# Kernel tuning notes

Hardware: AMD Instinct MI355X
Metric: run time of the kernel (lower is better)

Reference implementation:

```python
import jax, jax.numpy as jnp
import numpy as np

EPS = 1e-6

def rms_norm(x, w):
    x32 = x.astype(jnp.float32)
    y = x32 * jax.lax.rsqrt(jnp.mean(x32 * x32, axis=-1, keepdims=True) + EPS)
    return y.astype(x.dtype) * w

def setup_inputs() -> dict:
    key = jax.random.key(0)
    ks = jax.random.split(key, 12)
    V, Dm, S, Bz, L = 32000, 1024, 256, 2, 2048
    input_ids = jax.random.randint(ks[0], (Bz, L), 0, V)
    embedding = 0.02 * jax.random.normal(ks[1], (V, Dm), dtype=jnp.float32)
    embed_norm_w = jnp.ones((Dm,), dtype=jnp.float32)
    ssm_norm_w = jnp.ones((Dm,), dtype=jnp.float32)
    # A = 0.999 * exp(1j * theta): magnitude 0.999, random phase
    theta = jax.random.normal(ks[2], (S,), dtype=jnp.float32)
    A_re = 0.999 * jnp.cos(theta)
    A_im = 0.999 * jnp.sin(theta)
    # complex randn has real/imag parts with std 1/sqrt(2)
    cs = 1.0 / np.sqrt(2.0)
    B_re = cs * jax.random.normal(ks[3], (Dm, S), dtype=jnp.float32) / np.sqrt(S)
    B_im = cs * jax.random.normal(ks[4], (Dm, S), dtype=jnp.float32) / np.sqrt(S)
    C_re = cs * jax.random.normal(ks[5], (S, Dm), dtype=jnp.float32) / np.sqrt(S)
    C_im = cs * jax.random.normal(ks[6], (S, Dm), dtype=jnp.float32) / np.sqrt(S)
    D_p = jax.random.normal(ks[7], (Dm,), dtype=jnp.float32)
    head_w = jax.random.normal(ks[8], (Dm, V), dtype=jnp.float32) / np.sqrt(Dm)
    head_b = jnp.zeros((V,), dtype=jnp.float32)
    return dict(input_ids=input_ids, embedding=embedding, embed_norm_w=embed_norm_w,
                ssm_norm_w=ssm_norm_w, A_re=A_re, A_im=A_im, B_re=B_re, B_im=B_im,
                C_re=C_re, C_im=C_im, D_p=D_p, head_w=head_w, head_b=head_b)

def reference(input_ids, embedding, embed_norm_w, ssm_norm_w, A_re, A_im,
              B_re, B_im, C_re, C_im, D_p, head_w, head_b):
    # embed + RMSNorm
    x = rms_norm(embedding[input_ids], embed_norm_w)      # [B, L, D]
    # SSM input norm
    u = rms_norm(x, ssm_norm_w)                           # [B, L, D]
    L = u.shape[1]
    A = (A_re + 1j * A_im).astype(jnp.complex64)          # [S]
    Bc = (B_re + 1j * B_im).astype(jnp.complex64)         # [D, S]
    Cc = (C_re + 1j * C_im).astype(jnp.complex64)         # [S, D]
    # per-channel geometric kernel A^t, t = 0..L-1
    t = jnp.arange(L)[:, None]
    A_powers = A[None, :] ** t                            # [L, S] complex64
    uB = jnp.einsum('bli,iz->blz', u.astype(jnp.complex64), Bc)  # [B, L, S]
    # FFT-based causal convolution (fast_conv)
    T = 1 << int(np.ceil(np.log2(2 * L - 1)))
    Af = jnp.fft.fft(A_powers, n=T, axis=0)               # [T, S]
    Uf = jnp.fft.fft(uB, n=T, axis=1)                     # [B, T, S]
    xs = jnp.fft.ifft(Af[None, :, :] * Uf, axis=1)[:, :L]  # [B, L, S]
    y = jnp.real(jnp.einsum('blz,zo->blo', xs, Cc)) + D_p  # [B, L, D]
    return y @ head_w + head_b                            # [B, L, V]
```

## Files before the change

### kernel.cpp

```cpp
#include <hip/hip_runtime.h>

static __device__ __forceinline__ unsigned short f2bf(float f) {
  union { float f; unsigned u; } v; v.f = f;
  unsigned r = v.u + 0x7fffu + ((v.u >> 16) & 1u);
  return (unsigned short)(r >> 16);
}

struct alignas(8) us4 { unsigned short x, y, z, w; };

typedef __bf16 bf16x8 __attribute__((ext_vector_type(8)));
typedef float f32x4 __attribute__((ext_vector_type(4)));

static __device__ __forceinline__ void load_lds16(const void* g, void* l) {
  __builtin_amdgcn_global_load_lds(
      (const __attribute__((address_space(1))) unsigned int*)g,
      (__attribute__((address_space(3))) unsigned int*)l,
      16, 0, 0);
}

static __device__ __forceinline__ float block_sum(float v, float* sred) {
  #pragma unroll
  for (int o = 32; o > 0; o >>= 1) v += __shfl_down(v, o, 64);
  const int tid = threadIdx.x;
  __syncthreads();
  if ((tid & 63) == 0) sred[tid >> 6] = v;
  __syncthreads();
  return sred[0] + sred[1] + sred[2] + sred[3];
}

__global__ __launch_bounds__(256) void embed_norm(
    const int* __restrict__ ids, const float* __restrict__ emb,
    const float* __restrict__ w1, const float* __restrict__ w2,
    unsigned short* __restrict__ u_bf)
{
  __shared__ float sred[4];
  const int row = blockIdx.x;
  const int tid = threadIdx.x;
  const int id = ids[row];
  const float4 e = *(const float4*)(emb + (size_t)id * 1024 + tid * 4);
  float tot = block_sum(e.x*e.x + e.y*e.y + e.z*e.z + e.w*e.w, sred);
  float inv1 = rsqrtf(tot * (1.0f/1024.0f) + 1e-6f);
  const float4 a = *(const float4*)(w1 + tid * 4);
  float x0 = e.x*inv1*a.x, x1 = e.y*inv1*a.y, x2 = e.z*inv1*a.z, x3 = e.w*inv1*a.w;
  float tot2 = block_sum(x0*x0 + x1*x1 + x2*x2 + x3*x3, sred);
  float inv2 = rsqrtf(tot2 * (1.0f/1024.0f) + 1e-6f);
  const float4 b = *(const float4*)(w2 + tid * 4);
  us4 o;
  o.x = f2bf(x0*inv2*b.x); o.y = f2bf(x1*inv2*b.y);
  o.z = f2bf(x2*inv2*b.z); o.w = f2bf(x3*inv2*b.w);
  *(us4*)(u_bf + (size_t)row * 1024 + tid * 4) = o;
}

__global__ __launch_bounds__(256) void pack_B(
    const float* __restrict__ B_re, const float* __restrict__ B_im,
    unsigned short* __restrict__ BT)
{
  int t = blockIdx.x * 256 + threadIdx.x;
  int n = t >> 10, k = t & 1023;
  float v = (n < 256) ? B_re[(size_t)k * 256 + n] : B_im[(size_t)k * 256 + (n - 256)];
  BT[t] = f2bf(v);
}

__global__ __launch_bounds__(256) void pack_C(
    const float* __restrict__ C_re, const float* __restrict__ C_im,
    unsigned short* __restrict__ CT)
{
  int t = blockIdx.x * 256 + threadIdx.x;
  int d = t >> 9, sc = t & 511;
  float v = (sc < 256) ? C_re[(size_t)sc * 1024 + d] : -C_im[(size_t)(sc - 256) * 1024 + d];
  CT[t] = f2bf(v);
}

__global__ __launch_bounds__(256) void transpose_cvt(
    const float* __restrict__ in, unsigned short* __restrict__ out, int Kd, int Nd)
{
  __shared__ float tile[32][33];
  const int n0 = blockIdx.x * 32, k0 = blockIdx.y * 32;
  const int tx = threadIdx.x, ty = threadIdx.y;
  #pragma unroll
  for (int j = 0; j < 32; j += 8)
    tile[ty + j][tx] = in[(size_t)(k0 + ty + j) * Nd + n0 + tx];
  __syncthreads();
  #pragma unroll
  for (int j = 0; j < 32; j += 8)
    out[(size_t)(n0 + ty + j) * Kd + k0 + tx] = f2bf(tile[tx][ty + j]);
}

template<bool OUT_BF16, bool HAS_BIAS, bool NT_STORE>
__global__ __launch_bounds__(256) void gemm_bt(
    const unsigned short* __restrict__ A,
    const unsigned short* __restrict__ BT,
    const float* __restrict__ bias,
    void* __restrict__ outp,
    int M, int N, int K)
{
  __shared__ unsigned short As[128 * 32];
  __shared__ unsigned short Bs[128 * 32];
  const int tid = threadIdx.x;
  const int lane = tid & 63;
  const int wave = tid >> 6;

  const int nwg = gridDim.x;
  const int bid = blockIdx.x;
  const int q = nwg >> 3, r = nwg & 7;
  const int xcd = bid & 7, loc = bid >> 3;
  const int g = (xcd < r ? xcd * (q + 1) : r * (q + 1) + (xcd - r) * q) + loc;
  const int nMt = M >> 7;
  const int mt = g % nMt;
  const int nt = g / nMt;
  const int m0 = mt << 7;
  const int n0 = nt << 7;

  const int wm = (wave >> 1) * 64;
  const int wn = (wave & 1) * 64;

  f32x4 acc[4][4] = {};

  const int lin0 = wave * 64 + lane;
  const int rowS = lin0 >> 2;
  const int koS = (lin0 & 3) * 8;
  const int aq = lane >> 4;
  const int al = lane & 15;

  for (int k0 = 0; k0 < K; k0 += 32) {
    load_lds16(A  + (size_t)(m0 + rowS)      * K + k0 + koS, As + (size_t)lin0 * 8);
    load_lds16(A  + (size_t)(m0 + 64 + rowS) * K + k0 + koS, As + (size_t)(256 + lin0) * 8);
    load_lds16(BT + (size_t)(n0 + rowS)      * K + k0 + koS, Bs + (size_t)lin0 * 8);
    load_lds16(BT + (size_t)(n0 + 64 + rowS) * K + k0 + koS, Bs + (size_t)(256 + lin0) * 8);
    __syncthreads();
    const bf16x8* Ap = (const bf16x8*)As;
    const bf16x8* Bp = (const bf16x8*)Bs;
    bf16x8 af[4], bfr[4];
    #pragma unroll
    for (int i = 0; i < 4; ++i) af[i] = Ap[(wm + i * 16 + al) * 4 + aq];
    #pragma unroll
    for (int j = 0; j < 4; ++j) bfr[j] = Bp[(wn + j * 16 + al) * 4 + aq];
    #pragma unroll
    for (int i = 0; i < 4; ++i)
      #pragma unroll
      for (int j = 0; j < 4; ++j)
        acc[i][j] = __builtin_amdgcn_mfma_f32_16x16x32_bf16(af[i], bfr[j], acc[i][j], 0, 0, 0);
    __syncthreads();
  }

  const int row0 = m0 + wm + (lane >> 4) * 4;
  const int col0 = n0 + wn + al;
  #pragma unroll
  for (int j = 0; j < 4; ++j) {
    const int col = col0 + j * 16;
    float bv = 0.f;
    if (HAS_BIAS) bv = bias[col];
    #pragma unroll
    for (int i = 0; i < 4; ++i) {
      #pragma unroll
      for (int r2 = 0; r2 < 4; ++r2) {
        float v = acc[i][j][r2] + bv;
        size_t o = (size_t)(row0 + i * 16 + r2) * N + col;
        if (OUT_BF16) {
          ((unsigned short*)outp)[o] = f2bf(v);
        } else if (NT_STORE) {
          __builtin_nontemporal_store(v, (float*)outp + o);
        } else {
          ((float*)outp)[o] = v;
        }
      }
    }
  }
}

__global__ __launch_bounds__(256) void local_scan(
    float* __restrict__ xs, float* __restrict__ carry,
    const float* __restrict__ A_re, const float* __restrict__ A_im)
{
  int t = blockIdx.x * 256 + threadIdx.x;
  int s = t & 255;
  int chunk = (t >> 8) & 15;
  int b = t >> 12;
  float ar = A_re[s], ai = A_im[s];
  float xr = 0.f, xi = 0.f;
  size_t base = ((size_t)(b * 2048 + chunk * 128)) * 512 + s;
  for (int j = 0; j < 128; ++j) {
    float ur = xs[base], ui = xs[base + 256];
    float nr = fmaf(ar, xr, fmaf(-ai, xi, ur));
    float ni = fmaf(ar, xi, fmaf(ai, xr, ui));
    xs[base] = nr; xs[base + 256] = ni;
    xr = nr; xi = ni;
    base += 512;
  }
  int ci = (b * 16 + chunk) * 512 + s;
  carry[ci] = xr; carry[ci + 256] = xi;
}

__global__ __launch_bounds__(256) void carry_scan(
    const float* __restrict__ A_re, const float* __restrict__ A_im,
    const float* __restrict__ carry, float* __restrict__ state_before,
    float* __restrict__ Apow)
{
  int s = threadIdx.x;
  float ar = A_re[s], ai = A_im[s];
  float pr = 1.f, pi = 0.f;
  for (int t = 0; t <= 128; ++t) {
    Apow[t * 512 + s] = pr; Apow[t * 512 + 256 + s] = pi;
    float nr = pr * ar - pi * ai;
    float ni = pr * ai + pi * ar;
    pr = nr; pi = ni;
  }
  float cr = Apow[128 * 512 + s], ci = Apow[128 * 512 + 256 + s];
  for (int b = 0; b < 2; ++b) {
    float str = 0.f, sti = 0.f;
    for (int c = 0; c < 16; ++c) {
      int idx = (b * 16 + c) * 512 + s;
      state_before[idx] = str; state_before[idx + 256] = sti;
      float lr = carry[idx], li = carry[idx + 256];
      float nr = lr + cr * str - ci * sti;
      float ni = li + cr * sti + ci * str;
      str = nr; sti = ni;
    }
  }
}

__global__ __launch_bounds__(256) void combine_cast(
    const float* __restrict__ xs, const float* __restrict__ state_before,
    const float* __restrict__ Apow, unsigned short* __restrict__ xs_cat)
{
  int t = blockIdx.x * 256 + threadIdx.x;
  int s = t & 255, row = t >> 8;
  int l = row & 2047, b = row >> 11;
  int chunk = l >> 7, j = l & 127;
  size_t o = (size_t)row * 512 + s;
  float xr = xs[o], xi = xs[o + 256];
  int sbi = (b * 16 + chunk) * 512 + s;
  float sr = state_before[sbi], si = state_before[sbi + 256];
  int api = (j + 1) * 512 + s;
  float pr = Apow[api], pi = Apow[api + 256];
  float fr = xr + pr * sr - pi * si;
  float fi = xi + pr * si + pi * sr;
  xs_cat[o] = f2bf(fr); xs_cat[o + 256] = f2bf(fi);
}

extern "C" void kernel_launch(void* const* d_in, const int* in_sizes, int n_in,
                              void* d_out, int out_size, void* d_ws, size_t ws_size,
                              hipStream_t stream) {
  (void)in_sizes; (void)n_in; (void)out_size; (void)ws_size;
  const int*   ids    = (const int*)d_in[0];
  const float* emb    = (const float*)d_in[1];
  const float* w1     = (const float*)d_in[2];
  const float* w2     = (const float*)d_in[3];
  const float* A_re   = (const float*)d_in[4];
  const float* A_im   = (const float*)d_in[5];
  const float* B_re   = (const float*)d_in[6];
  const float* B_im   = (const float*)d_in[7];
  const float* C_re   = (const float*)d_in[8];
  const float* C_im   = (const float*)d_in[9];
  const float* D_p    = (const float*)d_in[10];
  const float* head_w = (const float*)d_in[11];
  const float* head_b = (const float*)d_in[12];
  float* out = (float*)d_out;

  char* ob = (char*)d_out;
  unsigned short* u_bf   = (unsigned short*)(ob + 0);
  unsigned short* BcatT  = (unsigned short*)(ob + 8388608);
  float* uBxs            = (float*)(ob + 9437184);
  float* carry           = (float*)(ob + 17825792);
  float* state_before    = (float*)(ob + 17891328);
  float* Apow            = (float*)(ob + 17956864);
  unsigned short* xs_cat = (unsigned short*)(ob + 18221056);
  unsigned short* CcatT  = (unsigned short*)(ob + 22415360);

  char* wb = (char*)d_ws;
  unsigned short* head_wT = (unsigned short*)(wb + 0);
  unsigned short* y_bf    = (unsigned short*)(wb + 65536000);

  embed_norm<<<4096, 256, 0, stream>>>(ids, emb, w1, w2, u_bf);
  pack_B<<<2048, 256, 0, stream>>>(B_re, B_im, BcatT);
  pack_C<<<2048, 256, 0, stream>>>(C_re, C_im, CcatT);
  transpose_cvt<<<dim3(1000, 32), dim3(32, 8), 0, stream>>>(head_w, head_wT, 1024, 32000);

  gemm_bt<false, false, false><<<128, 256, 0, stream>>>(u_bf, BcatT, nullptr, uBxs, 4096, 512, 1024);

  local_scan<<<32, 256, 0, stream>>>(uBxs, carry, A_re, A_im);
  carry_scan<<<1, 256, 0, stream>>>(A_re, A_im, carry, state_before, Apow);
  combine_cast<<<4096, 256, 0, stream>>>(uBxs, state_before, Apow, xs_cat);

  gemm_bt<true, true, false><<<256, 256, 0, stream>>>(xs_cat, CcatT, D_p, y_bf, 4096, 1024, 512);

  gemm_bt<false, true, true><<<8000, 256, 0, stream>>>(y_bf, head_wT, head_b, out, 4096, 32000, 1024);
}
```

Before: 1.084 ms.

## Add 256x256-tile double-buffered pipelined GEMM for the LM head

Introduces a new 512-thread GEMM kernel with 256x256 output tiles, 64-deep K steps, double-buffered LDS staging via global_load_lds, XOR-swizzled LDS reads, and interleaved load/MFMA phases with wave priority bumps. The large head projection (4096x32000x1024) now uses it instead of the 128x128 kernel, which raises operand reuse per loaded byte and overlaps memory traffic with compute. It also drops the nontemporal store path for the fp32 output. The risks are higher register and LDS pressure, which limits occupancy, and the loss of the nontemporal hint on the large output write.

```diff
diff --git a/kernel.cpp b/kernel.cpp
--- a/kernel.cpp
+++ b/kernel.cpp
@@ -86,7 +86,7 @@
     out[(size_t)(n0 + ty + j) * Kd + k0 + tx] = f2bf(tile[tx][ty + j]);
 }
 
-template<bool OUT_BF16, bool HAS_BIAS, bool NT_STORE>
+template<bool OUT_BF16, bool HAS_BIAS>
 __global__ __launch_bounds__(256) void gemm_bt(
     const unsigned short* __restrict__ A,
     const unsigned short* __restrict__ BT,
@@ -156,16 +156,195 @@
       for (int r2 = 0; r2 < 4; ++r2) {
         float v = acc[i][j][r2] + bv;
         size_t o = (size_t)(row0 + i * 16 + r2) * N + col;
-        if (OUT_BF16) {
-          ((unsigned short*)outp)[o] = f2bf(v);
-        } else if (NT_STORE) {
-          __builtin_nontemporal_store(v, (float*)outp + o);
-        } else {
-          ((float*)outp)[o] = v;
-        }
+        if (OUT_BF16) ((unsigned short*)outp)[o] = f2bf(v);
+        else          ((float*)outp)[o] = v;
       }
     }
   }
+}
+
+template<bool OUT_BF16, bool HAS_BIAS>
+__global__ __launch_bounds__(512, 2) void gemm256_bt(
+    const unsigned short* __restrict__ A,
+    const unsigned short* __restrict__ BT,
+    const float* __restrict__ bias,
+    void* __restrict__ outp,
+    int M, int N, int K)
+{
+  __shared__ unsigned short As[2][16384];
+  __shared__ unsigned short Bs[2][16384];
+  const int tid = threadIdx.x;
+  const int lane = tid & 63;
+  const int wave = tid >> 6;
+  const int wr = wave >> 2;
+  const int wc = wave & 3;
+
+  const int nwg = gridDim.x;
+  const int bid = blockIdx.x;
+  const int q8 = nwg >> 3, r8 = nwg & 7;
+  const int xcd = bid & 7, loc = bid >> 3;
+  const int g = (xcd < r8 ? xcd * (q8 + 1) : r8 * (q8 + 1) + (xcd - r8) * q8) + loc;
+  const int nMt = M >> 8;
+  const int mt = g % nMt, ntile = g / nMt;
+  const int m0 = mt << 8, n0 = ntile << 8;
+
+  const int s1i = tid + 512;
+  const int ra0 = tid >> 3, ra1 = s1i >> 3;
+  const size_t aoff0 = (size_t)ra0 * K + 8 * ((tid & 7) ^ (ra0 & 7));
+  const size_t aoff1 = (size_t)ra1 * K + 8 * ((s1i & 7) ^ (ra1 & 7));
+  const unsigned short* Ag0 = A + (size_t)m0 * K + aoff0;
+  const unsigned short* Ag1 = A + (size_t)m0 * K + aoff1;
+  const unsigned short* Bg0 = BT + (size_t)n0 * K + aoff0;
+  const unsigned short* Bg1 = BT + (size_t)n0 * K + aoff1;
+  const size_t hstep = (size_t)128 * K;
+
+  const int al = lane & 15, aq = lane >> 4;
+  const int arow = wr * 128 + al;
+  const int brow = wc * 64 + al;
+  const int sw0 = ((aq) ^ (al & 7)) << 4;
+  const int sw1 = ((4 + aq) ^ (al & 7)) << 4;
+
+  f32x4 acc[8][4] = {};
+  bf16x8 af[4][2];
+  bf16x8 bfr[4][2];
+
+  const int nT = K >> 6;
+
+#define STAGE_A_(b, h, tt) do { \
+    load_lds16(Ag0 + (size_t)(h) * hstep + (size_t)(tt) * 64, &As[b][(h) * 8192 + tid * 8]); \
+    load_lds16(Ag1 + (size_t)(h) * hstep + (size_t)(tt) * 64, &As[b][(h) * 8192 + 4096 + tid * 8]); \
+  } while (0)
+#define STAGE_B_(b, h, tt) do { \
+    load_lds16(Bg0 + (size_t)(h) * hstep + (size_t)(tt) * 64, &Bs[b][(h) * 8192 + tid * 8]); \
+    load_lds16(Bg1 + (size_t)(h) * hstep + (size_t)(tt) * 64, &Bs[b][(h) * 8192 + 4096 + tid * 8]); \
+  } while (0)
+#define DSRD_A_(b, ih) do { \
+    const char* p_ = (const char*)As[b] + ((size_t)(arow + (ih) * 64) << 7); \
+    af[0][0] = *(const bf16x8*)(p_ + sw0);        af[0][1] = *(const bf16x8*)(p_ + sw1); \
+    af[1][0] = *(const bf16x8*)(p_ + 2048 + sw0); af[1][1] = *(const bf16x8*)(p_ + 2048 + sw1); \
+    af[2][0] = *(const bf16x8*)(p_ + 4096 + sw0); af[2][1] = *(const bf16x8*)(p_ + 4096 + sw1); \
+    af[3][0] = *(const bf16x8*)(p_ + 6144 + sw0); af[3][1] = *(const bf16x8*)(p_ + 6144 + sw1); \
+  } while (0)
+#define DSRD_B_(b, jh) do { \
+    const char* p_ = (const char*)Bs[b] + ((size_t)(brow + (jh) * 32) << 7); \
+    bfr[(jh)*2+0][0] = *(const bf16x8*)(p_ + sw0);        bfr[(jh)*2+0][1] = *(const bf16x8*)(p_ + sw1); \
+    bfr[(jh)*2+1][0] = *(const bf16x8*)(p_ + 2048 + sw0); bfr[(jh)*2+1][1] = *(const bf16x8*)(p_ + 2048 + sw1); \
+  } while (0)
+#define MMA_Q_(ih, jh) do { \
+    _Pragma("unroll") for (int i_ = 0; i_ < 4; ++i_) { \
+      _Pragma("unroll") for (int j_ = 0; j_ < 2; ++j_) { \
+        f32x4 c_ = acc[(ih)*4+i_][(jh)*2+j_]; \
+        c_ = __builtin_amdgcn_mfma_f32_16x16x32_bf16(af[i_][0], bfr[(jh)*2+j_][0], c_, 0, 0, 0); \
+        c_ = __builtin_amdgcn_mfma_f32_16x16x32_bf16(af[i_][1], bfr[(jh)*2+j_][1], c_, 0, 0, 0); \
+        acc[(ih)*4+i_][(jh)*2+j_] = c_; \
+      } \
+    } \
+  } while (0)
+#define BARx() do { asm volatile("" ::: "memory"); __builtin_amdgcn_s_barrier(); asm volatile("" ::: "memory"); } while (0)
+#define VMW4() asm volatile("s_waitcnt vmcnt(4)" ::: "memory")
+#define VMW0() asm volatile("s_waitcnt vmcnt(0)" ::: "memory")
+#define PRIO1() __builtin_amdgcn_s_setprio(1)
+#define PRIO0() __builtin_amdgcn_s_setprio(0)
+
+  STAGE_A_(0, 0, 0); STAGE_A_(0, 1, 0);
+  STAGE_B_(0, 0, 0); STAGE_B_(0, 1, 0);
+  STAGE_B_(1, 0, 1); STAGE_B_(1, 1, 1);
+  VMW4();
+  BARx();
+
+  for (int t = 0; t + 3 < nT; t += 2) {
+    DSRD_A_(0, 0); DSRD_B_(0, 0);
+    STAGE_A_(1, 0, t + 1);
+    BARx(); PRIO1(); MMA_Q_(0, 0); PRIO0(); BARx();
+
+    DSRD_B_(0, 1);
+    STAGE_A_(1, 1, t + 1);
+    BARx(); PRIO1(); MMA_Q_(0, 1); PRIO0(); BARx();
+
+    DSRD_A_(0, 1);
+    STAGE_B_(0, 0, t + 2);
+    BARx(); PRIO1(); MMA_Q_(1, 0); PRIO0(); BARx();
+
+    STAGE_B_(0, 1, t + 2);
+    BARx(); PRIO1(); MMA_Q_(1, 1); PRIO0();
+    VMW4();
+    BARx();
+
+    DSRD_A_(1, 0); DSRD_B_(1, 0);
+    STAGE_A_(0, 0, t + 2);
+    BARx(); PRIO1(); MMA_Q_(0, 0); PRIO0(); BARx();
+
+    DSRD_B_(1, 1);
+    STAGE_A_(0, 1, t + 2);
+    BARx(); PRIO1(); MMA_Q_(0, 1); PRIO0(); BARx();
+
+    DSRD_A_(1, 1);
+    STAGE_B_(1, 0, t + 3);
+    BARx(); PRIO1(); MMA_Q_(1, 0); PRIO0(); BARx();
+
+    STAGE_B_(1, 1, t + 3);
+    BARx(); PRIO1(); MMA_Q_(1, 1); PRIO0();
+    VMW4();
+    BARx();
+  }
+
+  {
+    const int t = nT - 2;
+    DSRD_A_(0, 0); DSRD_B_(0, 0);
+    STAGE_A_(1, 0, t + 1);
+    BARx(); PRIO1(); MMA_Q_(0, 0); PRIO0(); BARx();
+
+    DSRD_B_(0, 1);
+    STAGE_A_(1, 1, t + 1);
+    BARx(); PRIO1(); MMA_Q_(0, 1); PRIO0(); BARx();
+
+    DSRD_A_(0, 1);
+    BARx(); PRIO1(); MMA_Q_(1, 0); PRIO0(); BARx();
+
+    BARx(); PRIO1(); MMA_Q_(1, 1); PRIO0();
+    VMW0();
+    BARx();
+
+    DSRD_A_(1, 0); DSRD_B_(1, 0);
+    BARx(); PRIO1(); MMA_Q_(0, 0); PRIO0(); BARx();
+
+    DSRD_B_(1, 1);
+    BARx(); PRIO1(); MMA_Q_(0, 1); PRIO0(); BARx();
+
+    DSRD_A_(1, 1);
+    BARx(); PRIO1(); MMA_Q_(1, 0); PRIO0(); BARx();
+
+    MMA_Q_(1, 1);
+  }
+
+  const int row0 = m0 + wr * 128 + (lane >> 4) * 4;
+  const int col0 = n0 + wc * 64 + al;
+  #pragma unroll
+  for (int j = 0; j < 4; ++j) {
+    const int col = col0 + j * 16;
+    float bv = 0.f;
+    if (HAS_BIAS) bv = bias[col];
+    #pragma unroll
+    for (int i = 0; i < 8; ++i) {
+      #pragma unroll
+      for (int r2 = 0; r2 < 4; ++r2) {
+        float v = acc[i][j][r2] + bv;
+        size_t o = (size_t)(row0 + i * 16 + r2) * N + col;
+        if (OUT_BF16) ((unsigned short*)outp)[o] = f2bf(v);
+        else          ((float*)outp)[o] = v;
+      }
+    }
+  }
+#undef STAGE_A_
+#undef STAGE_B_
+#undef DSRD_A_
+#undef DSRD_B_
+#undef MMA_Q_
+#undef BARx
+#undef VMW4
+#undef VMW0
+#undef PRIO1
+#undef PRIO0
 }
 
 __global__ __launch_bounds__(256) void local_scan(
@@ -276,13 +455,13 @@
   pack_C<<<2048, 256, 0, stream>>>(C_re, C_im, CcatT);
   transpose_cvt<<<dim3(1000, 32), dim3(32, 8), 0, stream>>>(head_w, head_wT, 1024, 32000);
 
-  gemm_bt<false, false, false><<<128, 256, 0, stream>>>(u_bf, BcatT, nullptr, uBxs, 4096, 512, 1024);
+  gemm_bt<false, false><<<128, 256, 0, stream>>>(u_bf, BcatT, nullptr, uBxs, 4096, 512, 1024);
 
   local_scan<<<32, 256, 0, stream>>>(uBxs, carry, A_re, A_im);
   carry_scan<<<1, 256, 0, stream>>>(A_re, A_im, carry, state_before, Apow);
   combine_cast<<<4096, 256, 0, stream>>>(uBxs, state_before, Apow, xs_cat);
 
-  gemm_bt<true, true, false><<<256, 256, 0, stream>>>(xs_cat, CcatT, D_p, y_bf, 4096, 1024, 512);
-
-  gemm_bt<false, true, true><<<8000, 256, 0, stream>>>(y_bf, head_wT, head_b, out, 4096, 32000, 1024);
-}
+  gemm_bt<true, true><<<256, 256, 0, stream>>>(xs_cat, CcatT, D_p, y_bf, 4096, 1024, 512);
+
+  gemm256_bt<false, true><<<2000, 512, 0, stream>>>(y_bf, head_wT, head_b, out, 4096, 32000, 1024);
+}
```

After: 1.060 ms. 1.02x faster.
